# Optimization experiments

Measured on AMD Instinct MI355X. Metric: run time of the kernel, lower is better.

## Reference

```python
import jax, jax.numpy as jnp
import numpy as np

LN_EPS = 1e-5


def _layernorm(h, g, b):
    mu = jnp.mean(h, axis=-1, keepdims=True)
    var = jnp.var(h, axis=-1, keepdims=True)
    return (h - mu) / jnp.sqrt(var + LN_EPS) * g + b


def setup_inputs() -> dict:
    key = jax.random.key(0)
    ks = jax.random.split(key, 16)
    B, N, C, T = 32, 1024, 64, 24
    K, Fc, Ft = 3, 64, 64

    def xav(k, shape):
        lim = (6.0 / (shape[-2] + shape[-1])) ** 0.5
        return jax.random.uniform(k, shape, jnp.float32, -lim, lim)

    return {
        "x": jax.random.normal(ks[0], (B, N, C, T), jnp.float32),
        "cheb": jax.random.normal(ks[1], (K, N, N), jnp.float32) / np.float32(N) ** 0.5,
        "U1": jax.random.uniform(ks[2], (N,), jnp.float32),
        "U2": xav(ks[3], (C, N)),
        "U3": jax.random.uniform(ks[4], (C,), jnp.float32),
        "b_e": xav(ks[5], (1, T, T)),
        "V_e": xav(ks[6], (T, T)),
        "W1": jax.random.uniform(ks[7], (T,), jnp.float32),
        "W2": xav(ks[8], (C, T)),
        "W3": jax.random.uniform(ks[9], (C,), jnp.float32),
        "b_s": xav(ks[10], (1, N, N)),
        "V_s": xav(ks[11], (N, N)),
        "Theta": xav(ks[12], (K, C, Fc)),
        "tc_w": jax.random.normal(ks[13], (Ft, Fc, 1, 3), jnp.float32) * 0.05,
        "tc_b": jnp.zeros((Ft,), jnp.float32),
        "rc_w": jax.random.normal(ks[14], (Ft, C, 1, 1), jnp.float32) * 0.05,
        "rc_b": jnp.zeros((Ft,), jnp.float32),
        "ln_g": jnp.ones((Ft,), jnp.float32),
        "ln_b": jnp.zeros((Ft,), jnp.float32),
    }


def reference(x, cheb, U1, U2, U3, b_e, V_e, W1, W2, W3, b_s, V_s,
              Theta, tc_w, tc_b, rc_w, rc_b, ln_g, ln_b):
    B, N, C, T = x.shape
    K = Theta.shape[0]

    # ---- temporal attention: E (B,T,T), softmax over axis 1 ----
    lhs_t = jnp.einsum('bnct,n->btc', x, U1) @ U2            # (B,T,N)
    rhs_t = jnp.einsum('c,bnct->bnt', U3, x)                 # (B,N,T)
    prod_t = jnp.einsum('btn,bnu->btu', lhs_t, rhs_t)        # (B,T,T)
    E = jnp.einsum('bik,jk->bij', jax.nn.sigmoid(prod_t + b_e), V_e)
    E = jax.nn.softmax(E, axis=1)

    # ---- apply temporal attention ----
    x_TAt = jnp.einsum('bft,btu->bfu', x.reshape(B, N * C, T), E)
    x_TAt = x_TAt.reshape(B, N, C, T)

    # ---- spatial attention: S (B,N,N), softmax over axis 1 ----
    lhs_s = jnp.einsum('bnct,t->bnc', x_TAt, W1) @ W2        # (B,N,T)
    rhs_s = jnp.einsum('c,bnct->btn', W3, x_TAt)             # (B,T,N)
    prod_s = jnp.einsum('bnt,btm->bnm', lhs_s, rhs_s)        # (B,N,N)
    S = jnp.einsum('bik,jk->bij', jax.nn.sigmoid(prod_s + b_s), V_s)
    S = jax.nn.softmax(S, axis=1)

    # ---- K-order Chebyshev conv with spatial attention ----
    out = jnp.zeros((B, N, Theta.shape[2], T), x.dtype)
    for k in range(K):
        Tk_at = cheb[k] * S                                   # (B,N,N)
        # rhs[b,i,c,t] = sum_m Tk_at[b,m,i] * x[b,m,c,t]
        rhs = jnp.einsum('bmi,bmct->bict', Tk_at, x)
        out = out + jnp.einsum('bict,cf->bift', rhs, Theta[k])
    spatial_gcn = jax.nn.relu(out)                            # (B,N,Fc,T)

    # ---- time conv (1x3, pad (0,1)) on (B,Fc,N,T) ----
    tci = jnp.transpose(spatial_gcn, (0, 2, 1, 3))            # (B,Fc,N,T)
    tco = jax.lax.conv_general_dilated(
        tci, tc_w, window_strides=(1, 1), padding=((0, 0), (1, 1)),
        dimension_numbers=('NCHW', 'OIHW', 'NCHW'))
    tco = tco + tc_b[None, :, None, None]
    tco = jnp.transpose(tco, (0, 2, 1, 3))                    # (B,N,Ft,T)

    # ---- residual 1x1 conv on raw x ----
    rci = jnp.transpose(x, (0, 2, 1, 3))                      # (B,C,N,T)
    rco = jax.lax.conv_general_dilated(
        rci, rc_w, window_strides=(1, 1), padding=((0, 0), (0, 0)),
        dimension_numbers=('NCHW', 'OIHW', 'NCHW'))
    rco = rco + rc_b[None, :, None, None]
    rco = jnp.transpose(rco, (0, 2, 1, 3))                    # (B,N,Ft,T)

    out = jax.nn.relu(rco + tco)                              # (B,N,Ft,T)
    out = _layernorm(jnp.transpose(out, (0, 1, 3, 2)), ln_g, ln_b)
    return jnp.transpose(out, (0, 1, 3, 2))                   # (B,N,Ft,T)
```

## Files before the change

### kernel.cpp

```cpp
#include <hip/hip_runtime.h>

typedef __attribute__((ext_vector_type(8))) short short8;
typedef __attribute__((ext_vector_type(4))) float f32x4;
typedef __attribute__((ext_vector_type(4))) unsigned short ushort4_;

constexpr int B_ = 32;
constexpr int N_ = 1024;
constexpr int C_ = 64;
constexpr int T_ = 24;
constexpr int F_ = 64;
constexpr int CT_ = C_ * T_;
constexpr int KS_ = 3072;

__device__ __forceinline__ float sigmoidf_(float x) {
    return 1.0f / (1.0f + __expf(-x));
}
__device__ __forceinline__ unsigned short f2b(float f) {
    union { float f; unsigned u; } v; v.f = f;
    unsigned r = v.u + 0x7FFFu + ((v.u >> 16) & 1u);
    return (unsigned short)(r >> 16);
}
__device__ __forceinline__ float b2f(unsigned short h) {
    union { unsigned u; float f; } v; v.u = ((unsigned)h) << 16; return v.f;
}
__device__ __forceinline__ void gload_lds16(const unsigned short* g, unsigned short* l) {
    __builtin_amdgcn_global_load_lds(
        (const __attribute__((address_space(1))) unsigned int*)g,
        (__attribute__((address_space(3))) unsigned int*)l, 16, 0, 0);
}

__global__ __launch_bounds__(256) void k_xreduce(const float* __restrict__ x,
        const float* __restrict__ U1, const float* __restrict__ U3,
        float* __restrict__ rhs_t, float* __restrict__ partial) {
    int b = blockIdx.y, g0 = blockIdx.x * 32;
    int tid = threadIdx.x;
    __shared__ float xr[8 * CT_];
    __shared__ float u3s[C_];
    if (tid < C_) u3s[tid] = U3[tid];
    float pacc[6] = {0, 0, 0, 0, 0, 0};
    for (int ph = 0; ph < 4; ++ph) {
        int n0 = g0 + ph * 8;
        __syncthreads();
        const float4* x4 = (const float4*)(x + ((size_t)(b * N_ + n0)) * CT_);
#pragma unroll
        for (int e = 0; e < 12; ++e) {
            int i4 = e * 256 + tid;
            float4 v = x4[i4];
            int i = i4 * 4;
            xr[i] = v.x; xr[i + 1] = v.y; xr[i + 2] = v.z; xr[i + 3] = v.w;
        }
        __syncthreads();
        if (tid < 192) {
            int n = tid / 24, t = tid % 24;
            const float* xn = xr + n * CT_ + t;
            float acc = 0.f;
#pragma unroll
            for (int c = 0; c < C_; ++c) acc += u3s[c] * xn[c * 24];
            rhs_t[((size_t)(b * N_ + n0 + n)) * T_ + t] = acc;
        }
#pragma unroll
        for (int n = 0; n < 8; ++n) {
            float u = U1[n0 + n];
            const float* xn = xr + n * CT_;
#pragma unroll
            for (int e = 0; e < 6; ++e) pacc[e] += u * xn[tid + e * 256];
        }
    }
    float* pp = partial + ((size_t)(b * 32 + blockIdx.x)) * CT_;
#pragma unroll
    for (int e = 0; e < 6; ++e) pp[tid + e * 256] = pacc[e];
}

__global__ void k_lhs_reduce(const float* __restrict__ partial, float* __restrict__ lhs_t0) {
    int idx = blockIdx.x * 256 + threadIdx.x;
    if (idx >= B_ * CT_) return;
    int b = idx / CT_, flat = idx % CT_;
    float acc = 0.f;
#pragma unroll
    for (int ch = 0; ch < 32; ++ch) acc += partial[((size_t)(b * 32 + ch)) * CT_ + flat];
    lhs_t0[idx] = acc;
}

__global__ void k_lhs_t(const float* __restrict__ lhs_t0, const float* __restrict__ U2,
                        float* __restrict__ lhs_t) {
    int idx = blockIdx.x * 256 + threadIdx.x;
    if (idx >= B_ * T_ * N_) return;
    int n2 = idx % N_;
    int t = (idx / N_) % T_;
    int b = idx / (T_ * N_);
    const float* l0 = lhs_t0 + (size_t)b * CT_;
    float acc = 0.f;
#pragma unroll
    for (int c = 0; c < C_; ++c) acc += l0[c * T_ + t] * U2[c * N_ + n2];
    lhs_t[idx] = acc;
}

__global__ __launch_bounds__(576) void k_prodt(const float* __restrict__ lhs_t,
        const float* __restrict__ rhs_t, float* __restrict__ ptp) {
    int b = blockIdx.y, ch = blockIdx.x;
    int tid = threadIdx.x;
    __shared__ float lt[24][128];
    __shared__ float rt[128][25];
    int n0 = ch * 128;
    for (int e = tid; e < 24 * 128; e += 576) {
        int i = e >> 7, nn = e & 127;
        lt[i][nn] = lhs_t[((size_t)b * T_ + i) * N_ + n0 + nn];
    }
    const float* rg = rhs_t + ((size_t)b * N_ + n0) * T_;
    for (int e = tid; e < 128 * 24; e += 576) {
        int nn = e / 24, t = e - nn * 24;
        rt[nn][t] = rg[e];
    }
    __syncthreads();
    int i = tid / 24, u = tid - (tid / 24) * 24;
    float acc = 0.f;
#pragma unroll 8
    for (int nn = 0; nn < 128; ++nn) acc += lt[i][nn] * rt[nn][u];
    ptp[(((size_t)b * 8 + ch) * 24 + i) * 24 + u] = acc;
}

__global__ void k_temporal_E(const float* __restrict__ ptp,
                             const float* __restrict__ b_e, const float* __restrict__ V_e,
                             float* __restrict__ E) {
    int b = blockIdx.x;
    int tid = threadIdx.x;
    int i = tid / T_, u = tid % T_;
    __shared__ float sig[T_][T_];
    __shared__ float e0s[T_][T_];
    __shared__ float mcol[T_], scol[T_];
    float acc = 0.f;
#pragma unroll
    for (int ch = 0; ch < 8; ++ch)
        acc += ptp[(((size_t)b * 8 + ch) * 24 + i) * 24 + u];
    sig[i][u] = sigmoidf_(acc + b_e[i * T_ + u]);
    __syncthreads();
    int j = u;
    float e0 = 0.f;
#pragma unroll
    for (int kk = 0; kk < T_; ++kk) e0 += sig[i][kk] * V_e[j * T_ + kk];
    e0s[i][j] = e0;
    __syncthreads();
    if (tid < T_) {
        float mx = -1e30f;
        for (int ii = 0; ii < T_; ++ii) mx = fmaxf(mx, e0s[ii][tid]);
        float s = 0.f;
        for (int ii = 0; ii < T_; ++ii) s += __expf(e0s[ii][tid] - mx);
        mcol[tid] = mx; scol[tid] = s;
    }
    __syncthreads();
    E[(size_t)b * T_ * T_ + i * T_ + j] = __expf(e0s[i][j] - mcol[j]) / scol[j];
}

__global__ __launch_bounds__(256) void k_tspatial(const float* __restrict__ x,
        const float* __restrict__ E, const float* __restrict__ W1g,
        const float* __restrict__ W2, const float* __restrict__ W3g,
        float* __restrict__ lhs_s, float* __restrict__ rhs_s,
        unsigned short* __restrict__ xTt) {
    int b = blockIdx.y;
    int n0 = blockIdx.x * 4;
    int tid = threadIdx.x;
    __shared__ float Es[T_ * T_];
    __shared__ float W1s[T_];
    __shared__ float W2s[C_ * T_];
    __shared__ float xr[4][64][25];
    __shared__ float l0s[4][64];
    for (int e = tid; e < T_ * T_; e += 256) Es[e] = E[(size_t)b * T_ * T_ + e];
    for (int e = tid; e < C_ * T_; e += 256) W2s[e] = W2[e];
    if (tid < T_) W1s[tid] = W1g[tid];
    size_t base = ((size_t)b * N_ + n0) * CT_;
    const float4* x4 = (const float4*)(x + base);
#pragma unroll
    for (int i = 0; i < 6; ++i) {
        int e4 = i * 256 + tid;
        float4 v = x4[e4];
        int e = e4 * 4;
        int nl = e / CT_; int rem = e - nl * CT_; int c = rem / 24; int tl = rem - c * 24;
        xr[nl][c][tl] = v.x; xr[nl][c][tl + 1] = v.y;
        xr[nl][c][tl + 2] = v.z; xr[nl][c][tl + 3] = v.w;
    }
    __syncthreads();
    int nl = tid >> 6, c = tid & 63;
    float xv[T_];
#pragma unroll
    for (int t = 0; t < T_; ++t) xv[t] = xr[nl][c][t];
#pragma unroll
    for (int i = 0; i < 24; ++i) {
        int idx = i * 256 + tid;
        int cc = idx & 63, nn = (idx >> 6) & 3, t = idx >> 8;
        xTt[((size_t)(b * T_ + t) * N_ + n0 + nn) * 64 + cc] = f2b(xr[nn][cc][t]);
    }
    float w3 = W3g[c];
    float u[T_];
#pragma unroll
    for (int j = 0; j < T_; ++j) {
        float a = 0.f;
#pragma unroll
        for (int t = 0; t < T_; ++t) a += xv[t] * Es[t * T_ + j];
        u[j] = a;
    }
    float l0 = 0.f;
#pragma unroll
    for (int j = 0; j < T_; ++j) l0 += u[j] * W1s[j];
    __syncthreads();
#pragma unroll
    for (int j = 0; j < T_; ++j) xr[nl][c][j] = w3 * u[j];
    l0s[nl][c] = l0;
    __syncthreads();
    if (tid < 4 * T_) {
        int t = tid % T_, g = tid / T_;
        float racc = 0.f, lacc = 0.f;
        for (int cc = 0; cc < 64; ++cc) {
            racc += xr[g][cc][t];
            lacc += l0s[g][cc] * W2s[cc * T_ + t];
        }
        rhs_s[((size_t)b * T_ + t) * N_ + n0 + g] = racc;
        lhs_s[((size_t)(b * N_ + n0 + g)) * T_ + t] = lacc;
    }
}

__global__ void k_cvt_bf(const float* __restrict__ v, unsigned short* __restrict__ o) {
    int i = blockIdx.x * 256 + threadIdx.x;
    o[i] = f2b(v[i]);
}

__global__ void k_wcat(const float* __restrict__ tc_w, const float* __restrict__ rc_w,
                       unsigned short* __restrict__ Wcat) {
    int i = blockIdx.x * 256 + threadIdx.x;
    if (i >= F_ * 256) return;
    int ft = i >> 8, k = i & 255;
    int sel = k >> 6, c = k & 63;
    float v = (sel < 3) ? tc_w[(ft * C_ + c) * 3 + sel] : rc_w[ft * C_ + c];
    Wcat[i] = f2b(v);
}

__global__ void k_thp(const float* __restrict__ Theta, unsigned short* __restrict__ Thp) {
    int i = blockIdx.x * 256 + threadIdx.x;
    if (i >= 192 * 64) return;
    int kf = i >> 6, c = i & 63;
    int k = kf >> 6, f = kf & 63;
    Thp[i] = f2b(Theta[((size_t)k * 64 + c) * 64 + f]);
}

__global__ __launch_bounds__(256) void k_sig(const float* __restrict__ lhs_s,
        const float* __restrict__ rhs_s, const float* __restrict__ b_s,
        unsigned short* __restrict__ sigA) {
    int b = blockIdx.z, i0 = blockIdx.y * 64, k0 = blockIdx.x * 256;
    int tid = threadIdx.x;
    __shared__ float lh[64 * T_];
    __shared__ float rh[T_][256];
    for (int e = tid; e < 64 * T_; e += 256) lh[e] = lhs_s[((size_t)b * N_ + i0) * T_ + e];
#pragma unroll
    for (int t = 0; t < T_; ++t) rh[t][tid] = rhs_s[((size_t)b * T_ + t) * N_ + k0 + tid];
    __syncthreads();
    int kg = k0 + tid;
    for (int ii = 0; ii < 64; ++ii) {
        float acc = b_s[(size_t)(i0 + ii) * N_ + kg];
#pragma unroll
        for (int t = 0; t < T_; ++t) acc += lh[ii * T_ + t] * rh[t][tid];
        sigA[((size_t)b * N_ + i0 + ii) * N_ + kg] = f2b(sigmoidf_(acc));
    }
}

__global__ __launch_bounds__(256) void k_yTmm(const unsigned short* __restrict__ xTt,
        const unsigned short* __restrict__ Thp, unsigned short* __restrict__ yT) {
    int bt = blockIdx.y;
    int b = bt / T_, t = bt - b * T_;
    int m0 = blockIdx.x * 128;
    int tid = threadIdx.x;
    int lane = tid & 63, wv = tid >> 6;
    __shared__ __align__(16) char smem[50688];
    unsigned short* Asb = (unsigned short*)smem;
    unsigned short* Bsb = (unsigned short*)(smem + 24576);
    unsigned short* Cl  = (unsigned short*)(smem + 24576);
#pragma unroll
    for (int e = 0; e < 6; ++e) {
        int chunk = e * 256 + tid;
        int row = chunk >> 3, slot = chunk & 7;
        int gslot = slot ^ (row & 7);
        gload_lds16(Thp + row * 64 + gslot * 8, &Asb[chunk * 8]);
    }
    const unsigned short* Bg = xTt + ((size_t)bt * N_ + m0) * 64;
#pragma unroll
    for (int e = 0; e < 4; ++e) {
        int chunk = e * 256 + tid;
        int row = chunk >> 3, slot = chunk & 7;
        int gslot = slot ^ (row & 7);
        gload_lds16(Bg + (size_t)row * 64 + gslot * 8, &Bsb[chunk * 8]);
    }
    __syncthreads();

    short8 bf[2][2];
#pragma unroll
    for (int ni = 0; ni < 2; ++ni)
#pragma unroll
        for (int kk = 0; kk < 2; ++kk) {
            int r = wv * 32 + ni * 16 + (lane & 15);
            int slot = (kk * 4 + (lane >> 4)) ^ (r & 7);
            bf[ni][kk] = *(const short8*)&Bsb[r * 64 + slot * 8];
        }
    f32x4 acc[12][2];
#pragma unroll
    for (int mi = 0; mi < 12; ++mi)
#pragma unroll
        for (int ni = 0; ni < 2; ++ni) acc[mi][ni] = (f32x4){0.f, 0.f, 0.f, 0.f};
#pragma unroll
    for (int mi = 0; mi < 12; ++mi) {
        short8 af[2];
#pragma unroll
        for (int kk = 0; kk < 2; ++kk) {
            int r = mi * 16 + (lane & 15);
            int slot = (kk * 4 + (lane >> 4)) ^ (r & 7);
            af[kk] = *(const short8*)&Asb[r * 64 + slot * 8];
        }
#pragma unroll
        for (int kk = 0; kk < 2; ++kk)
#pragma unroll
            for (int ni = 0; ni < 2; ++ni)
                acc[mi][ni] = __builtin_amdgcn_mfma_f32_16x16x32_bf16(
                    af[kk], bf[ni][kk], acc[mi][ni], 0, 0, 0);
    }
#pragma unroll
    for (int h = 0; h < 2; ++h) {
        __syncthreads();
#pragma unroll
        for (int mi2 = 0; mi2 < 6; ++mi2) {
            int mi = h * 6 + mi2;
#pragma unroll
            for (int r = 0; r < 4; ++r) {
                int row = mi2 * 16 + (lane >> 4) * 4 + r;
#pragma unroll
                for (int ni = 0; ni < 2; ++ni)
                    Cl[row * 136 + wv * 32 + ni * 16 + (lane & 15)] = f2b(acc[mi][ni][r]);
            }
        }
        __syncthreads();
#pragma unroll
        for (int e = 0; e < 6; ++e) {
            int idx = e * 256 + tid;
            int row = idx >> 4, seg = idx & 15;
            int kf = h * 96 + row;
            int k = kf >> 6, f = kf & 63;
            uint4 v = *(const uint4*)&Cl[row * 136 + seg * 8];
            *(uint4*)&yT[((size_t)b * CT_ + f * T_ + t) * KS_ + k * N_ + m0 + seg * 8] = v;
        }
    }
}

__global__ void k_smstats(const unsigned short* __restrict__ S, float2* __restrict__ mst) {
    int b = blockIdx.y;
    int jj = threadIdx.x % 64;
    int ig = threadIdx.x / 64;
    int j = blockIdx.x * 64 + jj;
    __shared__ float rm[4][64], rs[4][64];
    float m = -1e30f, s = 0.f;
    for (int i = ig; i < N_; i += 4) {
        float v = b2f(S[((size_t)b * N_ + i) * N_ + j]);
        float mn = fmaxf(m, v);
        s = s * __expf(m - mn) + __expf(v - mn);
        m = mn;
    }
    rm[ig][jj] = m; rs[ig][jj] = s;
    __syncthreads();
    if (ig == 0) {
        float M = rm[0][jj], SS = rs[0][jj];
#pragma unroll
        for (int g = 1; g < 4; ++g) {
            float mg = rm[g][jj];
            float mn = fmaxf(M, mg);
            SS = SS * __expf(M - mn) + rs[g][jj] * __expf(mg - mn);
            M = mn;
        }
        mst[(size_t)b * N_ + j] = make_float2(M, 1.f / SS);
    }
}

__global__ __launch_bounds__(256) void k_chebSt(const unsigned short* __restrict__ chb,
        const unsigned short* __restrict__ S, const float2* __restrict__ mst,
        unsigned short* __restrict__ cs) {
    int b = blockIdx.z, i0 = blockIdx.y * 64, m0 = blockIdx.x * 64;
    int tid = threadIdx.x;
    __shared__ float st[64][65];
    __shared__ float cb[64][65];
    __shared__ float2 sst[64];
    if (tid < 64) sst[tid] = mst[(size_t)b * N_ + i0 + tid];
#pragma unroll
    for (int e = 0; e < 4; ++e) {
        int idx4 = e * 256 + tid;
        int mm = idx4 >> 4, ii0 = (idx4 & 15) * 4;
        ushort4_ v = *(const ushort4_*)&S[((size_t)b * N_ + m0 + mm) * N_ + i0 + ii0];
        st[mm][ii0] = b2f(v.x); st[mm][ii0 + 1] = b2f(v.y);
        st[mm][ii0 + 2] = b2f(v.z); st[mm][ii0 + 3] = b2f(v.w);
    }
    for (int k = 0; k < 3; ++k) {
        __syncthreads();
#pragma unroll
        for (int e = 0; e < 4; ++e) {
            int idx4 = e * 256 + tid;
            int mm = idx4 >> 4, ii0 = (idx4 & 15) * 4;
            ushort4_ v = *(const ushort4_*)&chb[((size_t)k * N_ + m0 + mm) * N_ + i0 + ii0];
            cb[mm][ii0] = b2f(v.x); cb[mm][ii0 + 1] = b2f(v.y);
            cb[mm][ii0 + 2] = b2f(v.z); cb[mm][ii0 + 3] = b2f(v.w);
        }
        __syncthreads();
#pragma unroll
        for (int e = 0; e < 16; ++e) {
            int idx = e * 256 + tid; int mm = idx & 63, ii = idx >> 6;
            float sm = __expf(st[mm][ii] - sst[ii].x) * sst[ii].y;
            cs[((size_t)b * N_ + i0 + ii) * KS_ + k * N_ + m0 + mm] =
                f2b(sm * cb[mm][ii]);
        }
    }
}

__global__ __launch_bounds__(512, 2) void k_gemm256(
        const unsigned short* __restrict__ A, long lda, long sA,
        const unsigned short* __restrict__ Bt, long ldb, long sB,
        void* __restrict__ Cc, long ldc, long sC, int K, int nbx, int nby, int obf) {
    __shared__ __align__(16) unsigned short As[2][256 * 64];
    __shared__ __align__(16) unsigned short Bs[2][256 * 64];
    int tid = threadIdx.x;
    int lane = tid & 63, w = tid >> 6;
    int wy = w >> 2, wx = w & 3;

    int nwg = gridDim.x;
    int cpx = nwg >> 3;
    int logical = (blockIdx.x & 7) * cpx + (blockIdx.x >> 3);
    int tpb = nbx * nby;
    int b = logical / tpb;
    int tile = logical % tpb;
    int i0 = (tile / nbx) * 256;
    int j0 = (tile % nbx) * 256;

    const unsigned short* Ab = A + (size_t)b * sA + (size_t)i0 * lda;
    const unsigned short* Bb = Bt + (size_t)b * sB + (size_t)j0 * ldb;

    auto STAGE = [&](int kt, int d) {
        int kof = kt << 6;
#pragma unroll
        for (int e = 0; e < 4; ++e) {
            int chunk = e * 512 + tid;
            int row = chunk >> 3, slot = chunk & 7;
            int gslot = slot ^ (row & 7);
            gload_lds16(Ab + (size_t)row * lda + kof + gslot * 8, &As[d][chunk * 8]);
        }
#pragma unroll
        for (int e = 0; e < 4; ++e) {
            int chunk = e * 512 + tid;
            int row = chunk >> 3, slot = chunk & 7;
            int gslot = slot ^ (row & 7);
            gload_lds16(Bb + (size_t)row * ldb + kof + gslot * 8, &Bs[d][chunk * 8]);
        }
    };
    auto READF = [&](short8* af, short8* bfv,
                     const unsigned short* Asb, const unsigned short* Bsb, int kkb) {
#pragma unroll
        for (int mi = 0; mi < 8; ++mi) {
            int r = wy * 128 + mi * 16 + (lane & 15);
            int slot = (kkb + (lane >> 4)) ^ (r & 7);
            af[mi] = *(const short8*)&Asb[r * 64 + slot * 8];
        }
#pragma unroll
        for (int ni = 0; ni < 4; ++ni) {
            int r = wx * 64 + ni * 16 + (lane & 15);
            int slot = (kkb + (lane >> 4)) ^ (r & 7);
            bfv[ni] = *(const short8*)&Bsb[r * 64 + slot * 8];
        }
    };

    f32x4 acc[8][4];
#pragma unroll
    for (int mi = 0; mi < 8; ++mi)
#pragma unroll
        for (int ni = 0; ni < 4; ++ni) acc[mi][ni] = (f32x4){0.f, 0.f, 0.f, 0.f};

    int nt = K >> 6;
    STAGE(0, 0);
    STAGE(1, 1);
    asm volatile("s_waitcnt vmcnt(8)" ::: "memory");
    __builtin_amdgcn_s_barrier();
    __builtin_amdgcn_sched_barrier(0);

    short8 a0[8], b0[4], a1[8], b1[4];
    READF(a0, b0, As[0], Bs[0], 0);

    for (int kt = 0; kt < nt; ++kt) {
        int cur = kt & 1;
        READF(a1, b1, As[cur], Bs[cur], 4);
        __builtin_amdgcn_s_setprio(1);
#pragma unroll
        for (int mi = 0; mi < 8; ++mi)
#pragma unroll
            for (int ni = 0; ni < 4; ++ni)
                acc[mi][ni] = __builtin_amdgcn_mfma_f32_16x16x32_bf16(
                    a0[mi], b0[ni], acc[mi][ni], 0, 0, 0);
        __builtin_amdgcn_s_setprio(0);
        asm volatile("s_waitcnt lgkmcnt(0)" ::: "memory");
        __builtin_amdgcn_sched_barrier(0);
        __builtin_amdgcn_s_barrier();
        __builtin_amdgcn_sched_barrier(0);
        if (kt + 2 < nt) STAGE(kt + 2, cur);
        __builtin_amdgcn_sched_barrier(0);
        __builtin_amdgcn_s_setprio(1);
#pragma unroll
        for (int mi = 0; mi < 8; ++mi)
#pragma unroll
            for (int ni = 0; ni < 4; ++ni)
                acc[mi][ni] = __builtin_amdgcn_mfma_f32_16x16x32_bf16(
                    a1[mi], b1[ni], acc[mi][ni], 0, 0, 0);
        __builtin_amdgcn_s_setprio(0);
        if (kt + 2 < nt) {
            asm volatile("s_waitcnt vmcnt(8)" ::: "memory");
        } else {
            asm volatile("s_waitcnt vmcnt(0)" ::: "memory");
        }
        __builtin_amdgcn_s_barrier();
        __builtin_amdgcn_sched_barrier(0);
        if (kt + 1 < nt)
            READF(a0, b0, As[cur ^ 1], Bs[cur ^ 1], 0);
    }

    if (obf) {
        unsigned short* Cb = (unsigned short*)Cc + (size_t)b * sC;
#pragma unroll
        for (int mi = 0; mi < 8; ++mi) {
#pragma unroll
            for (int r = 0; r < 4; ++r) {
                int i = i0 + wy * 128 + mi * 16 + (lane >> 4) * 4 + r;
                unsigned short* cp = Cb + (size_t)i * ldc + j0 + wx * 64 + (lane & 15);
#pragma unroll
                for (int ni = 0; ni < 4; ++ni) cp[ni * 16] = f2b(acc[mi][ni][r]);
            }
        }
    } else {
        float* Cb = (float*)Cc + (size_t)b * sC;
#pragma unroll
        for (int mi = 0; mi < 8; ++mi) {
#pragma unroll
            for (int r = 0; r < 4; ++r) {
                int i = i0 + wy * 128 + mi * 16 + (lane >> 4) * 4 + r;
                float* cp = Cb + (size_t)i * ldc + j0 + wx * 64 + (lane & 15);
#pragma unroll
                for (int ni = 0; ni < 4; ++ni) cp[ni * 16] = acc[mi][ni][r];
            }
        }
    }
}

__global__ __launch_bounds__(256) void k_final(const float* __restrict__ x,
        const void* __restrict__ sgin, int sbf, const unsigned short* __restrict__ Wcat,
        const float* __restrict__ tc_b, const float* __restrict__ rc_b,
        const float* __restrict__ ln_g, const float* __restrict__ ln_b,
        float* __restrict__ out) {
    int b = blockIdx.y;
    int n0 = blockIdx.x * 4;
    int tid = threadIdx.x;
    int lane = tid & 63, wv = tid >> 6;

    __shared__ __align__(16) char smem[25600];
    unsigned short* sgb = (unsigned short*)smem;
    unsigned short* xb  = (unsigned short*)(smem + 13312);
    float* Cl = (float*)smem;
    __shared__ float tbs[64], gs[64], bbs[64];
    __shared__ float mus[96], rss[96];

    if (tid < 64) {
        tbs[tid] = tc_b[tid] + rc_b[tid];
        gs[tid] = ln_g[tid];
        bbs[tid] = ln_b[tid];
    }
    for (int e = tid; e < 512; e += 256) {
        int nl = e >> 7, r = (e >> 6) & 1, c = e & 63;
        int tt = r ? 25 : 0;
        sgb[(nl * 26 + tt) * 64 + (((c >> 3) ^ (tt & 7)) << 3) + (c & 7)] = 0;
    }
    size_t base = ((size_t)b * N_ + n0) * CT_;
    const float4* xg4 = (const float4*)(x + base);
#pragma unroll
    for (int i = 0; i < 6; ++i) {
        int e4 = i * 256 + tid;
        float4 xv4 = xg4[e4];
        int e = e4 * 4;
        int nl = e / CT_;
        int rem = e - nl * CT_;
        int c = rem / 24;
        int tl = rem - c * 24;
        float xv[4] = {xv4.x, xv4.y, xv4.z, xv4.w};
#pragma unroll
        for (int j = 0; j < 4; ++j) {
            int tj = tl + j;
            xb[(nl * 24 + tj) * 64 + (((c >> 3) ^ (tj & 7)) << 3) + (c & 7)] = f2b(xv[j]);
        }
    }
    if (sbf) {
        const uint4* sg8 = (const uint4*)((const unsigned short*)sgin + base);
#pragma unroll
        for (int i = 0; i < 3; ++i) {
            int e8 = i * 256 + tid;
            uint4 v = sg8[e8];
            const unsigned short* sp = (const unsigned short*)&v;
            int e = e8 * 8;
            int nl = e / CT_;
            int rem = e - nl * CT_;
            int c = rem / 24;
            int tl = rem - c * 24;
#pragma unroll
            for (int j = 0; j < 8; ++j) {
                int tt = tl + j + 1;
                unsigned short sb = sp[j];
                sgb[(nl * 26 + tt) * 64 + (((c >> 3) ^ (tt & 7)) << 3) + (c & 7)] =
                    (sb & 0x8000u) ? (unsigned short)0 : sb;
            }
        }
    } else {
        const float4* sg4 = (const float4*)((const float*)sgin + base);
#pragma unroll
        for (int i = 0; i < 6; ++i) {
            int e4 = i * 256 + tid;
            float4 sv4 = sg4[e4];
            int e = e4 * 4;
            int nl = e / CT_;
            int rem = e - nl * CT_;
            int c = rem / 24;
            int tl = rem - c * 24;
            float sv[4] = {sv4.x, sv4.y, sv4.z, sv4.w};
#pragma unroll
            for (int j = 0; j < 4; ++j) {
                int tt = tl + j + 1;
                sgb[(nl * 26 + tt) * 64 + (((c >> 3) ^ (tt & 7)) << 3) + (c & 7)] =
                    f2b(fmaxf(sv[j], 0.f));
            }
        }
    }

    int ft = wv * 16 + (lane & 15);
    int g4 = lane >> 4;
    short8 bfr[8];
#pragma unroll
    for (int ks = 0; ks < 8; ++ks)
        bfr[ks] = *(const short8*)&Wcat[ft * 256 + ks * 32 + g4 * 8];

    int rnl[6], rt[6];
#pragma unroll
    for (int mi = 0; mi < 6; ++mi) {
        int row = mi * 16 + (lane & 15);
        rnl[mi] = row / 24;
        rt[mi] = row - rnl[mi] * 24;
    }

    __syncthreads();

    f32x4 acc[6];
#pragma unroll
    for (int mi = 0; mi < 6; ++mi) acc[mi] = (f32x4){0.f, 0.f, 0.f, 0.f};
#pragma unroll
    for (int mi = 0; mi < 6; ++mi) {
        int nl = rnl[mi], t = rt[mi];
#pragma unroll
        for (int ks = 0; ks < 8; ++ks) {
            const int sel = ks >> 1;
            int slot = (ks & 1) * 4 + g4;
            short8 af;
            if (sel < 3) {
                int tt = t + sel;
                af = *(const short8*)&sgb[(nl * 26 + tt) * 64 + ((slot ^ (tt & 7)) << 3)];
            } else {
                af = *(const short8*)&xb[(nl * 24 + t) * 64 + ((slot ^ (t & 7)) << 3)];
            }
            acc[mi] = __builtin_amdgcn_mfma_f32_16x16x32_bf16(af, bfr[ks], acc[mi], 0, 0, 0);
        }
    }

    __syncthreads();
#pragma unroll
    for (int mi = 0; mi < 6; ++mi)
#pragma unroll
        for (int r = 0; r < 4; ++r)
            Cl[(mi * 16 + (lane >> 4) * 4 + r) * 66 + wv * 16 + (lane & 15)] = acc[mi][r];
    __syncthreads();

    if (tid < 96) {
        float s = 0.f, s2 = 0.f;
#pragma unroll
        for (int f = 0; f < 64; ++f) {
            float v = fmaxf(Cl[tid * 66 + f] + tbs[f], 0.f);
            s += v; s2 += v * v;
        }
        float mu = s * (1.f / 64.f);
        float var = s2 * (1.f / 64.f) - mu * mu;
        mus[tid] = mu;
        rss[tid] = rsqrtf(var + 1e-5f);
    }
    __syncthreads();

    float4* o4 = (float4*)(out + base);
#pragma unroll
    for (int i = 0; i < 6; ++i) {
        int e4 = i * 256 + tid;
        int e = e4 * 4;
        int nl = e / CT_;
        int rem = e - nl * CT_;
        int f = rem / 24;
        int t0v = rem - f * 24;
        float g = gs[f], bb2 = bbs[f], tb2 = tbs[f];
        float vals[4];
#pragma unroll
        for (int j = 0; j < 4; ++j) {
            int row = nl * 24 + t0v + j;
            float v = fmaxf(Cl[row * 66 + f] + tb2, 0.f);
            vals[j] = (v - mus[row]) * rss[row] * g + bb2;
        }
        float4 r;
        r.x = vals[0]; r.y = vals[1]; r.z = vals[2]; r.w = vals[3];
        o4[e4] = r;
    }
}

extern "C" void kernel_launch(void* const* d_in, const int* in_sizes, int n_in,
                              void* d_out, int out_size, void* d_ws, size_t ws_size,
                              hipStream_t stream) {
    const float* x    = (const float*)d_in[0];
    const float* cheb = (const float*)d_in[1];
    const float* U1   = (const float*)d_in[2];
    const float* U2   = (const float*)d_in[3];
    const float* U3   = (const float*)d_in[4];
    const float* b_e  = (const float*)d_in[5];
    const float* V_e  = (const float*)d_in[6];
    const float* W1   = (const float*)d_in[7];
    const float* W2   = (const float*)d_in[8];
    const float* W3   = (const float*)d_in[9];
    const float* b_s  = (const float*)d_in[10];
    const float* V_s  = (const float*)d_in[11];
    const float* Theta= (const float*)d_in[12];
    const float* tc_w = (const float*)d_in[13];
    const float* tc_b = (const float*)d_in[14];
    const float* rc_w = (const float*)d_in[15];
    const float* rc_b = (const float*)d_in[16];
    const float* ln_g = (const float*)d_in[17];
    const float* ln_b = (const float*)d_in[18];
    float* out = (float*)d_out;

    char* base = (char*)d_ws;
    size_t o = 0;
    auto alloc = [&](size_t bytes) { size_t r = o; o += (bytes + 255) & ~(size_t)255; return r; };
    float* lhs_t   = (float*)(base + alloc((size_t)B_ * T_ * N_ * 4));
    float* rhs_t   = (float*)(base + alloc((size_t)B_ * N_ * T_ * 4));
    float* Ebuf    = (float*)(base + alloc((size_t)B_ * T_ * T_ * 4));
    float* partial = (float*)(base + alloc((size_t)B_ * 32 * CT_ * 4));
    float* ptp     = (float*)(base + alloc((size_t)B_ * 8 * T_ * T_ * 4));
    float* lhs_t0  = (float*)(base + alloc((size_t)B_ * CT_ * 4));
    float* lhs_s   = (float*)(base + alloc((size_t)B_ * N_ * T_ * 4));
    float* rhs_s   = (float*)(base + alloc((size_t)B_ * T_ * N_ * 4));
    unsigned short* V_sb = (unsigned short*)(base + alloc((size_t)N_ * N_ * 2));
    unsigned short* Wcat = (unsigned short*)(base + alloc((size_t)F_ * 256 * 2));
    unsigned short* Thp  = (unsigned short*)(base + alloc((size_t)192 * 64 * 2));
    unsigned short* chb  = (unsigned short*)(base + alloc((size_t)3 * N_ * N_ * 2));
    float2* mstats = (float2*)(base + alloc((size_t)B_ * N_ * 8));
    size_t regA = alloc((size_t)B_ * N_ * KS_ * 2);
    size_t regB = alloc((size_t)B_ * CT_ * KS_ * 2);
    unsigned short* xTt    = (unsigned short*)(base + regA);
    unsigned short* chebSt = (unsigned short*)(base + regA);
    unsigned short* sigA   = (unsigned short*)(base + regB);
    unsigned short* yT     = (unsigned short*)(base + regB);
    unsigned short* Sb = (unsigned short*)out;

    size_t gcn_bytes = (size_t)B_ * N_ * CT_ * 2;
    int use_aux = (ws_size >= o + gcn_bytes + 256) ? 1 : 0;
    unsigned short* gcnb = use_aux ? (unsigned short*)(base + alloc(gcn_bytes)) : nullptr;
    void* gcn_ptr = use_aux ? (void*)gcnb : (void*)out;
    const void* sgin = use_aux ? (const void*)gcnb : (const void*)out;

    dim3 b256(256);
    k_cvt_bf<<<dim3(N_ * N_ / 256), b256, 0, stream>>>(V_s, V_sb);
    k_cvt_bf<<<dim3(3 * N_ * N_ / 256), b256, 0, stream>>>(cheb, chb);
    k_wcat<<<dim3((F_ * 256 + 255) / 256), b256, 0, stream>>>(tc_w, rc_w, Wcat);
    k_thp<<<dim3((192 * 64 + 255) / 256), b256, 0, stream>>>(Theta, Thp);
    k_xreduce<<<dim3(N_ / 32, B_), b256, 0, stream>>>(x, U1, U3, rhs_t, partial);
    k_lhs_reduce<<<dim3((B_ * CT_ + 255) / 256), b256, 0, stream>>>(partial, lhs_t0);
    k_lhs_t<<<dim3((B_ * T_ * N_) / 256), b256, 0, stream>>>(lhs_t0, U2, lhs_t);
    k_prodt<<<dim3(8, B_), dim3(576), 0, stream>>>(lhs_t, rhs_t, ptp);
    k_temporal_E<<<dim3(B_), dim3(576), 0, stream>>>(ptp, b_e, V_e, Ebuf);
    k_tspatial<<<dim3(N_ / 4, B_), b256, 0, stream>>>(x, Ebuf, W1, W2, W3,
                                                      lhs_s, rhs_s, xTt);
    k_sig<<<dim3(N_ / 256, N_ / 64, B_), b256, 0, stream>>>(lhs_s, rhs_s, b_s, sigA);
    k_gemm256<<<dim3(B_ * 4 * 4), dim3(512), 0, stream>>>(
        sigA, N_, (long)N_ * N_, V_sb, N_, 0, Sb, N_, (long)N_ * N_, N_, 4, 4, 1);
    k_smstats<<<dim3(N_ / 64, B_), b256, 0, stream>>>(Sb, mstats);
    k_yTmm<<<dim3(N_ / 128, B_ * T_), b256, 0, stream>>>(xTt, Thp, yT);
    k_chebSt<<<dim3(N_ / 64, N_ / 64, B_), b256, 0, stream>>>(chb, Sb, mstats, chebSt);
    k_gemm256<<<dim3(B_ * 4 * 6), dim3(512), 0, stream>>>(
        chebSt, KS_, (long)N_ * KS_, yT, KS_, (long)CT_ * KS_,
        gcn_ptr, CT_, (long)N_ * CT_, KS_, 6, 4, use_aux);
    k_final<<<dim3(N_ / 4, B_), b256, 0, stream>>>(x, sgin, use_aux, Wcat, tc_b, rc_b,
                                                   ln_g, ln_b, out);
}
```

Before: 993.4 us.

## Double-buffer full k-tile fragments in registers and unroll GEMM main loop by two

The 256x256 bf16 GEMM main loop now loads every LDS fragment for the next 64-wide k-tile into a second register set while the MFMAs for the current tile run. This replaces the old split of half-tile reads interleaved with the MFMAs. The loop is unrolled by two so the two fragment sets swap without copies. Launch bounds drop to one block per CU, freeing registers for the larger fragment set, which may cost latency hiding between workgroups. The loop also assumes an even number of k-tiles.

```diff
diff --git a/kernel.cpp b/kernel.cpp
--- a/kernel.cpp
+++ b/kernel.cpp
@@ -412,7 +412,7 @@
     }
 }
 
-__global__ __launch_bounds__(512, 2) void k_gemm256(
+__global__ __launch_bounds__(512, 1) void k_gemm256(
         const unsigned short* __restrict__ A, long lda, long sA,
         const unsigned short* __restrict__ Bt, long ldb, long sB,
         void* __restrict__ Cc, long ldc, long sC, int K, int nbx, int nby, int obf) {
@@ -451,19 +451,33 @@
             gload_lds16(Bb + (size_t)row * ldb + kof + gslot * 8, &Bs[d][chunk * 8]);
         }
     };
-    auto READF = [&](short8* af, short8* bfv,
-                     const unsigned short* Asb, const unsigned short* Bsb, int kkb) {
+
+    struct Frag { short8 a0[8]; short8 b0[4]; short8 a1[8]; short8 b1[4]; };
+    auto RD = [&](Frag& f, const unsigned short* Asb, const unsigned short* Bsb)
+            __attribute__((always_inline)) {
 #pragma unroll
         for (int mi = 0; mi < 8; ++mi) {
             int r = wy * 128 + mi * 16 + (lane & 15);
-            int slot = (kkb + (lane >> 4)) ^ (r & 7);
-            af[mi] = *(const short8*)&Asb[r * 64 + slot * 8];
+            int slot = (lane >> 4) ^ (r & 7);
+            f.a0[mi] = *(const short8*)&Asb[r * 64 + slot * 8];
         }
 #pragma unroll
         for (int ni = 0; ni < 4; ++ni) {
             int r = wx * 64 + ni * 16 + (lane & 15);
-            int slot = (kkb + (lane >> 4)) ^ (r & 7);
-            bfv[ni] = *(const short8*)&Bsb[r * 64 + slot * 8];
+            int slot = (lane >> 4) ^ (r & 7);
+            f.b0[ni] = *(const short8*)&Bsb[r * 64 + slot * 8];
+        }
+#pragma unroll
+        for (int mi = 0; mi < 8; ++mi) {
+            int r = wy * 128 + mi * 16 + (lane & 15);
+            int slot = (4 + (lane >> 4)) ^ (r & 7);
+            f.a1[mi] = *(const short8*)&Asb[r * 64 + slot * 8];
+        }
+#pragma unroll
+        for (int ni = 0; ni < 4; ++ni) {
+            int r = wx * 64 + ni * 16 + (lane & 15);
+            int slot = (4 + (lane >> 4)) ^ (r & 7);
+            f.b1[ni] = *(const short8*)&Bsb[r * 64 + slot * 8];
         }
     };
 
@@ -473,50 +487,65 @@
 #pragma unroll
         for (int ni = 0; ni < 4; ++ni) acc[mi][ni] = (f32x4){0.f, 0.f, 0.f, 0.f};
 
+    auto MFMA64 = [&](Frag& f) __attribute__((always_inline)) {
+        __builtin_amdgcn_s_setprio(1);
+#pragma unroll
+        for (int mi = 0; mi < 8; ++mi)
+#pragma unroll
+            for (int ni = 0; ni < 4; ++ni)
+                acc[mi][ni] = __builtin_amdgcn_mfma_f32_16x16x32_bf16(
+                    f.a0[mi], f.b0[ni], acc[mi][ni], 0, 0, 0);
+#pragma unroll
+        for (int mi = 0; mi < 8; ++mi)
+#pragma unroll
+            for (int ni = 0; ni < 4; ++ni)
+                acc[mi][ni] = __builtin_amdgcn_mfma_f32_16x16x32_bf16(
+                    f.a1[mi], f.b1[ni], acc[mi][ni], 0, 0, 0);
+        __builtin_amdgcn_s_setprio(0);
+    };
+
     int nt = K >> 6;
+    int cur = 0;
+    Frag fA, fB;
+
     STAGE(0, 0);
     STAGE(1, 1);
     asm volatile("s_waitcnt vmcnt(8)" ::: "memory");
+    __builtin_amdgcn_sched_barrier(0);
     __builtin_amdgcn_s_barrier();
     __builtin_amdgcn_sched_barrier(0);
-
-    short8 a0[8], b0[4], a1[8], b1[4];
-    READF(a0, b0, As[0], Bs[0], 0);
-
-    for (int kt = 0; kt < nt; ++kt) {
-        int cur = kt & 1;
-        READF(a1, b1, As[cur], Bs[cur], 4);
-        __builtin_amdgcn_s_setprio(1);
-#pragma unroll
-        for (int mi = 0; mi < 8; ++mi)
-#pragma unroll
-            for (int ni = 0; ni < 4; ++ni)
-                acc[mi][ni] = __builtin_amdgcn_mfma_f32_16x16x32_bf16(
-                    a0[mi], b0[ni], acc[mi][ni], 0, 0, 0);
-        __builtin_amdgcn_s_setprio(0);
-        asm volatile("s_waitcnt lgkmcnt(0)" ::: "memory");
+    RD(fA, As[0], Bs[0]);
+    asm volatile("s_waitcnt lgkmcnt(0)" ::: "memory");
+    __builtin_amdgcn_sched_barrier(0);
+    __builtin_amdgcn_s_barrier();
+    __builtin_amdgcn_sched_barrier(0);
+
+    auto ITER = [&](int kt, Frag& fc, Frag& fn) __attribute__((always_inline)) {
+        bool stg = (kt + 2 < nt);
+        bool nxt = (kt + 1 < nt);
+        if (stg) STAGE(kt + 2, cur);
         __builtin_amdgcn_sched_barrier(0);
-        __builtin_amdgcn_s_barrier();
-        __builtin_amdgcn_sched_barrier(0);
-        if (kt + 2 < nt) STAGE(kt + 2, cur);
-        __builtin_amdgcn_sched_barrier(0);
-        __builtin_amdgcn_s_setprio(1);
-#pragma unroll
-        for (int mi = 0; mi < 8; ++mi)
-#pragma unroll
-            for (int ni = 0; ni < 4; ++ni)
-                acc[mi][ni] = __builtin_amdgcn_mfma_f32_16x16x32_bf16(
-                    a1[mi], b1[ni], acc[mi][ni], 0, 0, 0);
-        __builtin_amdgcn_s_setprio(0);
-        if (kt + 2 < nt) {
-            asm volatile("s_waitcnt vmcnt(8)" ::: "memory");
-        } else {
-            asm volatile("s_waitcnt vmcnt(0)" ::: "memory");
-        }
-        __builtin_amdgcn_s_barrier();
-        __builtin_amdgcn_sched_barrier(0);
-        if (kt + 1 < nt)
-            READF(a0, b0, As[cur ^ 1], Bs[cur ^ 1], 0);
+        if (nxt) {
+            if (stg) { asm volatile("s_waitcnt vmcnt(8)" ::: "memory"); }
+            else     { asm volatile("s_waitcnt vmcnt(0)" ::: "memory"); }
+            __builtin_amdgcn_sched_barrier(0);
+            __builtin_amdgcn_s_barrier();
+            __builtin_amdgcn_sched_barrier(0);
+            RD(fn, As[cur ^ 1], Bs[cur ^ 1]);
+        }
+        MFMA64(fc);
+        if (nxt) {
+            asm volatile("s_waitcnt lgkmcnt(0)" ::: "memory");
+            __builtin_amdgcn_sched_barrier(0);
+            __builtin_amdgcn_s_barrier();
+            __builtin_amdgcn_sched_barrier(0);
+            cur ^= 1;
+        }
+    };
+
+    for (int kt = 0; kt < nt; kt += 2) {
+        ITER(kt, fA, fB);
+        ITER(kt + 1, fB, fA);
     }
 
     if (obf) {
```

Result: slower. 3.110 ms (+213.0%).
